# Kernel optimization log

Measured on AMD Instinct MI355X. Metric: run time of the kernel, lower is better.

Reference implementation:

```python
import jax, jax.numpy as jnp
import numpy as np

D_MODEL = 2048
N_HEADS = 16
N_KV_HEADS = 4
D_HEAD = 128
MAX_SEQ_LEN = 4096
RANK = 32
GAMMA_INIT = 0.05
ROPE_BASE = 10000.0


def setup_inputs() -> dict:
    key = jax.random.key(0)
    ks = jax.random.split(key, 10)
    B, T = 1, 2048
    s = lambda fan_in: 1.0 / np.sqrt(fan_in)
    x = jax.random.normal(ks[0], (B, T, D_MODEL), dtype=jnp.float32)
    Wq = jax.random.normal(ks[1], (D_MODEL, N_HEADS * D_HEAD), dtype=jnp.float32) * s(D_MODEL)
    Wk = jax.random.normal(ks[2], (D_MODEL, N_KV_HEADS * D_HEAD), dtype=jnp.float32) * s(D_MODEL)
    Wv = jax.random.normal(ks[3], (D_MODEL, N_KV_HEADS * D_HEAD), dtype=jnp.float32) * s(D_MODEL)
    Wo = jax.random.normal(ks[4], (N_HEADS * D_HEAD, D_MODEL), dtype=jnp.float32) * s(N_HEADS * D_HEAD)
    pol_dir = jax.random.normal(ks[5], (N_HEADS,), dtype=jnp.float32) * 0.1
    pol_WA = jax.random.normal(ks[6], (D_MODEL, RANK), dtype=jnp.float32) * s(D_MODEL)
    pol_WB = jax.random.normal(ks[7], (D_MODEL, RANK), dtype=jnp.float32) * s(D_MODEL)
    pol_gate = jnp.full((N_HEADS,), -3.0, dtype=jnp.float32)
    # gtp_gamma initialized so softplus(gtp_gamma) == geometric ALiBi-style gamma schedule
    slopes = np.linspace(3.0, -3.0, N_HEADS)
    gamma_t = np.clip(GAMMA_INIT * 2.0 ** slopes, 1e-4, None)
    gtp_gamma = jnp.asarray(np.log(np.expm1(gamma_t)), dtype=jnp.float32)
    return {"x": x, "Wq": Wq, "Wk": Wk, "Wv": Wv, "Wo": Wo,
            "pol_dir": pol_dir, "pol_WA": pol_WA, "pol_WB": pol_WB,
            "pol_gate": pol_gate, "gtp_gamma": gtp_gamma}


def _rope(x, offset=0):
    # x: [B,H,T,D]; standard rotate-half RoPE
    B, H, T, D = x.shape
    inv_freq = 1.0 / (ROPE_BASE ** (jnp.arange(0, D, 2, dtype=jnp.float32) / D))
    pos = jnp.arange(T, dtype=jnp.float32) + offset
    ang = pos[:, None] * inv_freq[None, :]          # [T, D/2]
    cos = jnp.cos(ang)[None, None]                  # [1,1,T,D/2]
    sin = jnp.sin(ang)[None, None]
    x1, x2 = x[..., : D // 2], x[..., D // 2 :]
    return jnp.concatenate([x1 * cos - x2 * sin, x2 * cos + x1 * sin], axis=-1)


def reference(x, Wq, Wk, Wv, Wo, pol_dir, pol_WA, pol_WB, pol_gate, gtp_gamma):
    B, T, _ = x.shape
    H, Hkv, D = N_HEADS, N_KV_HEADS, D_HEAD
    n_rep = H // Hkv
    Q = (x @ Wq).reshape(B, T, H, D).transpose(0, 2, 1, 3)     # [B,H,T,D]
    K = (x @ Wk).reshape(B, T, Hkv, D).transpose(0, 2, 1, 3)   # [B,Hkv,T,D]
    V = (x @ Wv).reshape(B, T, Hkv, D).transpose(0, 2, 1, 3)
    Q = _rope(Q)
    K = _rope(K)
    K = jnp.repeat(K, n_rep, axis=1)                           # [B,H,T,D]
    V = jnp.repeat(V, n_rep, axis=1)

    # ---- attention bias ----
    idx = jnp.arange(T)
    delta = (idx[:, None] - idx[None, :]).astype(jnp.float32)  # [T,T], i - j
    causal = delta >= 0
    pol = jnp.clip(pol_dir, -1.0, 1.0)
    polarity_bias = -pol[:, None, None] * (delta / float(MAX_SEQ_LEN))[None]     # [H,T,T]
    gamma = jnp.maximum(jax.nn.softplus(gtp_gamma), 1e-6)
    gtp_bias = -gamma[:, None, None] * jnp.maximum(delta, 0.0)[None]             # [H,T,T]
    bias = (polarity_bias + gtp_bias)[None]                                      # [1,H,T,T]
    # low-rank content-dependent sigmoid bilinear term (prefill: q_len == k_len)
    A = x @ pol_WA                                                               # [B,T,r]
    Bm = x @ pol_WB                                                              # [B,T,r]
    M = jax.nn.sigmoid(jnp.einsum('bir,bjr->bij', A, Bm))                        # [B,T,T]
    gate = jax.nn.sigmoid(pol_gate)[None, :, None, None]
    bias = bias + gate * M[:, None]                                              # [B,H,T,T]
    neg_inf = jnp.finfo(bias.dtype).min
    bias = jnp.where(causal[None, None], bias, neg_inf)

    # ---- SDPA ----
    scores = jnp.einsum('bhid,bhjd->bhij', Q, K) / jnp.sqrt(jnp.float32(D)) + bias
    attn = jax.nn.softmax(scores, axis=-1)
    out = jnp.einsum('bhij,bhjd->bhid', attn, V)                                 # [B,H,T,D]
    out = out.transpose(0, 2, 1, 3).reshape(B, T, H * D)
    return out @ Wo
```

## Files before the change

### kernel.cpp

```cpp
#include <hip/hip_runtime.h>
#include <math.h>

typedef short bf16x8 __attribute__((ext_vector_type(8)));
typedef float f32x4  __attribute__((ext_vector_type(4)));

#define MFMA16 __builtin_amdgcn_mfma_f32_16x16x32_bf16
#define LOG2E 1.4426950408889634f

static __device__ __forceinline__ short f2bf(float f) {
  union { float f; unsigned u; } x; x.f = f;
  unsigned r = (x.u + 0x7FFFu + ((x.u >> 16) & 1u)) >> 16;
  return (short)r;
}
static __device__ __forceinline__ unsigned packbf(float a, float b) {
  return (unsigned)(unsigned short)f2bf(a) | ((unsigned)(unsigned short)f2bf(b) << 16);
}
static __device__ __forceinline__ float bf2f(short s) {
  union { unsigned u; float f; } x; x.u = ((unsigned)(unsigned short)s) << 16;
  return x.f;
}
static __device__ __forceinline__ void gload_lds16(const void* g, void* l) {
  __builtin_amdgcn_global_load_lds((const __attribute__((address_space(1))) void*)g,
                                   (__attribute__((address_space(3))) void*)l, 16, 0, 0);
}
static __device__ __forceinline__ float ex2(float x) {
  float r; asm("v_exp_f32 %0, %1" : "=v"(r) : "v"(x)); return r;
}
static __device__ __forceinline__ float rcpf(float x) {
  float r; asm("v_rcp_f32 %0, %1" : "=v"(r) : "v"(x)); return r;
}
static __device__ __forceinline__ unsigned cvtpk(float lo, float hi) {
  unsigned r; asm("v_cvt_pk_bf16_f32 %0, %1, %2" : "=v"(r) : "v"(lo), "v"(hi));
  return r;
}

__device__ __forceinline__ void tr_tile(
    const float* __restrict__ in, short* __restrict__ out,
    int K, int N, int nt, int kt, float (*t)[33])
{
  int n0 = nt * 32, k0 = kt * 32;
  int tx = threadIdx.x & 31, ty = threadIdx.x >> 5;
  #pragma unroll
  for (int i = 0; i < 4; ++i)
    t[ty + 8 * i][tx] = in[(size_t)(k0 + ty + 8 * i) * N + n0 + tx];
  __syncthreads();
  #pragma unroll
  for (int i = 0; i < 4; ++i)
    out[(size_t)(n0 + ty + 8 * i) * K + k0 + tx] = f2bf(t[tx][ty + 8 * i]);
}

__global__ __launch_bounds__(256) void prep_kernel(
    const float* __restrict__ x, const float* __restrict__ Wq,
    const float* __restrict__ Wk, const float* __restrict__ Wv,
    const float* __restrict__ WA, const float* __restrict__ WB,
    short* __restrict__ xb, short* __restrict__ Wqt, short* __restrict__ Wkt,
    short* __restrict__ Wvt, short* __restrict__ WABt)
{
  __shared__ float t[32][33];
  int b = blockIdx.x;
  if (b < 4096)       tr_tile(Wq, Wqt, 2048, 2048, b & 63, b >> 6, t);
  else if (b < 5120)  { int c = b - 4096; tr_tile(Wk, Wkt, 2048, 512, c & 15, c >> 4, t); }
  else if (b < 6144)  { int c = b - 5120; tr_tile(Wv, Wvt, 2048, 512, c & 15, c >> 4, t); }
  else if (b < 6208)  { int c = b - 6144; tr_tile(WA, WABt, 2048, 32, 0, c, t); }
  else if (b < 6272)  { int c = b - 6208; tr_tile(WB, WABt + 32 * 2048, 2048, 32, 0, c, t); }
  else {
    int i = (b - 6272) * 256 + threadIdx.x;
    float4 v = ((const float4*)x)[i];
    short4 o; o.x = f2bf(v.x); o.y = f2bf(v.y); o.z = f2bf(v.z); o.w = f2bf(v.w);
    ((short4*)xb)[i] = o;
  }
}

__global__ __launch_bounds__(256) void mid_kernel(
    const float* __restrict__ Wo, short* __restrict__ Wot,
    short* __restrict__ Q, short* __restrict__ K)
{
  __shared__ float t[32][33];
  int b = blockIdx.x;
  if (b < 4096) { tr_tile(Wo, Wot, 2048, 2048, b & 63, b >> 6, t); return; }
  int idx = (b - 4096) * 256 + threadIdx.x;
  int d  = idx & 63;
  int hh = (idx >> 6) % 20;
  int tt = idx / (20 * 64);
  short* base = (hh < 16) ? Q + (size_t)tt * 2048 + hh * 128 + d
                          : K + (size_t)tt * 512 + (hh - 16) * 128 + d;
  float inv = __expf((float)d * -0.14391156831212789f);
  float ang = (float)tt * inv;
  float sn, cs;
  __sincosf(ang, &sn, &cs);
  float x1 = bf2f(base[0]), x2 = bf2f(base[64]);
  base[0]  = f2bf(x1 * cs - x2 * sn);
  base[64] = f2bf(x2 * cs + x1 * sn);
}

__device__ __forceinline__ void gemm128_core(
    const short* __restrict__ A, const short* __restrict__ Bt,
    int m0, int n0, int Kd, short* Asm, short* Bsm, f32x4 acc[4][4])
{
  const int tid = threadIdx.x;
  const int lane = tid & 63, w = tid >> 6;
  const int lr = lane & 15, g4 = lane >> 4;
  const int wm = w >> 1, wn = w & 1;

  for (int k0 = 0; k0 < Kd; k0 += 32) {
    #pragma unroll
    for (int s = 0; s < 2; ++s) {
      int c = (s * 4 + w) * 64 + lane;
      int row = c >> 2, q = c & 3;
      gload_lds16(A  + (size_t)(m0 + row) * Kd + k0 + q * 8,
                  Asm + (size_t)(s * 4 + w) * 64 * 8);
      gload_lds16(Bt + (size_t)(n0 + row) * Kd + k0 + q * 8,
                  Bsm + (size_t)(s * 4 + w) * 64 * 8);
    }
    __syncthreads();
    bf16x8 af[4], bff[4];
    #pragma unroll
    for (int mi = 0; mi < 4; ++mi)
      af[mi] = *(const bf16x8*)(Asm + (wm * 64 + mi * 16 + lr) * 32 + g4 * 8);
    #pragma unroll
    for (int ni = 0; ni < 4; ++ni)
      bff[ni] = *(const bf16x8*)(Bsm + (wn * 64 + ni * 16 + lr) * 32 + g4 * 8);
    #pragma unroll
    for (int mi = 0; mi < 4; ++mi)
      #pragma unroll
      for (int ni = 0; ni < 4; ++ni)
        acc[mi][ni] = MFMA16(af[mi], bff[ni], acc[mi][ni], 0, 0, 0);
    __syncthreads();
  }
}

__global__ __launch_bounds__(256, 3) void gemm_qkv_kernel(
    const short* __restrict__ xb, const short* __restrict__ Wqt,
    const short* __restrict__ Wkt, const short* __restrict__ Wvt,
    const short* __restrict__ WABt,
    short* __restrict__ Qb, short* __restrict__ Kb, short* __restrict__ Vtb,
    short* __restrict__ Ab, short* __restrict__ Bb)
{
  __shared__ __align__(16) short Asm[128 * 32];
  __shared__ __align__(16) short Bsm[128 * 32];
  f32x4 acc[4][4];
  #pragma unroll
  for (int i = 0; i < 4; ++i)
    #pragma unroll
    for (int j = 0; j < 4; ++j) acc[i][j] = (f32x4){0.f, 0.f, 0.f, 0.f};

  const int bx = blockIdx.x, by = blockIdx.y;
  const short* Bt; int mode, nl0;
  if (bx < 16)      { Bt = Wqt;  nl0 = bx * 128;        mode = 0; }
  else if (bx < 20) { Bt = Wkt;  nl0 = (bx - 16) * 128; mode = 1; }
  else if (bx < 24) { Bt = Wvt;  nl0 = (bx - 20) * 128; mode = 2; }
  else              { Bt = WABt; nl0 = 0;               mode = 3; }

  gemm128_core(xb, Bt, by * 128, nl0, 2048, Asm, Bsm, acc);

  const int tid = threadIdx.x, lane = tid & 63, w = tid >> 6;
  const int lr = lane & 15, g4 = lane >> 4, wm = w >> 1, wn = w & 1;
  #pragma unroll
  for (int mi = 0; mi < 4; ++mi) {
    #pragma unroll
    for (int ni = 0; ni < 4; ++ni) {
      int mb = by * 128 + wm * 64 + mi * 16 + g4 * 4;
      int nc = nl0 + wn * 64 + ni * 16 + lr;
      if (mode == 0) {
        #pragma unroll
        for (int r = 0; r < 4; ++r)
          Qb[(size_t)(mb + r) * 2048 + nc] = f2bf(acc[mi][ni][r]);
      } else if (mode == 1) {
        #pragma unroll
        for (int r = 0; r < 4; ++r)
          Kb[(size_t)(mb + r) * 512 + nc] = f2bf(acc[mi][ni][r]);
      } else if (mode == 2) {
        uint2 uu;
        uu.x = packbf(acc[mi][ni][0], acc[mi][ni][1]);
        uu.y = packbf(acc[mi][ni][2], acc[mi][ni][3]);
        *(uint2*)(Vtb + (size_t)nc * 2048 + mb) = uu;
      } else {
        if (wn == 0) {
          int col = ni * 16 + lr;
          #pragma unroll
          for (int r = 0; r < 4; ++r) {
            float sv = acc[mi][ni][r];
            if (col < 32) {
              Ab[(size_t)(mb + r) * 32 + col] = f2bf(sv * LOG2E);
            } else {
              Bb[(size_t)(mb + r) * 32 + (col - 32)] = f2bf(sv);
            }
          }
        }
      }
    }
  }
}

__global__ __launch_bounds__(256, 3) void gemm_out_kernel(
    const short* __restrict__ AO, const short* __restrict__ Wot,
    float* __restrict__ out)
{
  __shared__ __align__(16) short Asm[128 * 32];
  __shared__ __align__(16) short Bsm[128 * 32];
  f32x4 acc[4][4];
  #pragma unroll
  for (int i = 0; i < 4; ++i)
    #pragma unroll
    for (int j = 0; j < 4; ++j) acc[i][j] = (f32x4){0.f, 0.f, 0.f, 0.f};

  gemm128_core(AO, Wot, blockIdx.y * 128, blockIdx.x * 128, 2048, Asm, Bsm, acc);

  const int tid = threadIdx.x, lane = tid & 63, w = tid >> 6;
  const int lr = lane & 15, g4 = lane >> 4, wm = w >> 1, wn = w & 1;
  #pragma unroll
  for (int mi = 0; mi < 4; ++mi)
    #pragma unroll
    for (int ni = 0; ni < 4; ++ni) {
      int mb = blockIdx.y * 128 + wm * 64 + mi * 16 + g4 * 4;
      int nc = blockIdx.x * 128 + wn * 64 + ni * 16 + lr;
      #pragma unroll
      for (int r = 0; r < 4; ++r)
        out[(size_t)(mb + r) * 2048 + nc] = acc[mi][ni][r];
    }
}

__global__ __launch_bounds__(256, 2) void attn_kernel(
    const short* __restrict__ Qg, const short* __restrict__ Kg,
    const short* __restrict__ Vtg, const short* __restrict__ Ag,
    const short* __restrict__ Bg, const float* __restrict__ pol_dir,
    const float* __restrict__ pol_gate, const float* __restrict__ gtp_gamma,
    short* __restrict__ AO)
{
  __shared__ __align__(16) char lds[67584];
  char* const Vs = lds + 32768;
  char* const Ps = lds + 49152;

  const int tid = threadIdx.x;
  const int lane = tid & 63, w = tid >> 6;
  const int lr = lane & 15, g4 = lane >> 4;
  const int h  = blockIdx.x;
  const int by = blockIdx.y;
  const int qt = (by < 16) ? (31 - by) : (by - 16);
  const int q0 = qt * 64;
  const int kvh = h >> 2;
  const short* Kh = Kg + kvh * 128;
  const short* Vh = Vtg + (size_t)(kvh * 128) * 2048;

  float pol   = fminf(fmaxf(pol_dir[h], -1.f), 1.f);
  float gamma = fmaxf(log1pf(__expf(gtp_gamma[h])), 1e-6f);
  float gate  = (1.f / (1.f + __expf(-pol_gate[h]))) * LOG2E;
  const float c_h  = -(pol * (1.f / 4096.f) + gamma) * LOG2E;
  const float c16  = 16.f * c_h;
  const float chr1 = c_h, chr2 = c_h + c_h, chr3 = chr2 + c_h;
  const float sc = 0.08838834764831845f * LOG2E;
  const f32x4 z4 = {0.f, 0.f, 0.f, 0.f};

  #pragma unroll
  for (int s = 0; s < 4; ++s) {
    int idx = (w * 4 + s) * 64 + lane;
    int row = idx >> 4, slot = idx & 15;
    gload_lds16(Kh + (size_t)row * 512 + (slot ^ (row & 7)) * 8,
                lds + (w * 4 + s) * 1024);
  }
  #pragma unroll
  for (int s = 0; s < 4; ++s) {
    int idx = (w * 4 + s) * 64 + lane;
    int row = idx >> 3, slot = idx & 7;
    gload_lds16(Vh + (size_t)row * 2048 + (slot ^ (row & 7)) * 8,
                Vs + (w * 4 + s) * 1024);
  }
  #pragma unroll
  for (int s = 0; s < 4; ++s) {
    int c = tid + s * 256;
    int row = c >> 4, sl = c & 15;
    int4 v = *(const int4*)(Qg + (size_t)(q0 + row) * 2048 + h * 128 + sl * 8);
    *(int4*)(lds + 16384 + row * 256 + ((sl * 16) ^ ((row & 7) << 4))) = v;
  }
  {
    int row = tid >> 2, sl = tid & 3;
    int4 va = *(const int4*)(Ag + (size_t)(q0 + row) * 32 + sl * 8);
    *(int4*)(Ps + row * 80 + sl * 16) = va;
    int4 vb = *(const int4*)(Bg + (size_t)row * 32 + sl * 8);
    *(int4*)(lds + 57344 + row * 80 + sl * 16) = vb;
  }
  asm volatile("s_waitcnt vmcnt(0) lgkmcnt(0)" ::: "memory");
  __builtin_amdgcn_s_barrier();

  bf16x8 qf[4];
  #pragma unroll
  for (int kk = 0; kk < 4; ++kk)
    qf[kk] = *(const bf16x8*)(lds + 16384 + (w * 16 + lr) * 256 +
                              ((kk * 64 + g4 * 16) ^ ((lr & 7) << 4)));
  bf16x8 afr = *(const bf16x8*)(Ps + (w * 16 + lr) * 80 + g4 * 16);
  asm volatile("s_waitcnt lgkmcnt(0)" ::: "memory");
  __builtin_amdgcn_s_barrier();

  f32x4 acc_o[8];
  #pragma unroll
  for (int i = 0; i < 8; ++i) acc_o[i] = z4;
  float m_st = -INFINITY, l_st = 0.f;
  char* Pw = Ps + w * 2048;

  for (int jt = 0; jt <= qt; ++jt) {
    const int j0 = jt * 64;
    const bool pf = (jt < qt);
    char* Kcur = lds + ((jt & 1) << 14);
    char* Knxt = lds + (((jt + 1) & 1) << 14);
    char* Bcur = lds + 57344 + (jt & 1) * 5120;
    char* Bnxt = lds + 57344 + ((jt + 1) & 1) * 5120;

    int4 breg;
    if (pf) {
      int brow = tid >> 2, bsl = tid & 3;
      breg = *(const int4*)(Bg + (size_t)(j0 + 64 + brow) * 32 + bsl * 8);
      #pragma unroll
      for (int s = 0; s < 4; ++s) {
        int idx = (w * 4 + s) * 64 + lane;
        int row = idx >> 4, slot = idx & 15;
        gload_lds16(Kh + (size_t)(j0 + 64 + row) * 512 + (slot ^ (row & 7)) * 8,
                    Knxt + (w * 4 + s) * 1024);
      }
    }

    f32x4 acc_s[4], md4[4];
    __builtin_amdgcn_s_setprio(1);
    #pragma unroll
    for (int cb = 0; cb < 4; ++cb) {
      acc_s[cb] = z4;
      #pragma unroll
      for (int kk = 0; kk < 4; ++kk) {
        bf16x8 kf = *(const bf16x8*)(Kcur + (cb * 16 + lr) * 256 +
                                     ((kk * 64 + g4 * 16) ^ ((lr & 7) << 4)));
        acc_s[cb] = MFMA16(kf, qf[kk], acc_s[cb], 0, 0, 0);
      }
      bf16x8 bmf = *(const bf16x8*)(Bcur + (cb * 16 + lr) * 80 + g4 * 16);
      md4[cb] = MFMA16(bmf, afr, z4, 0, 0, 0);
    }
    __builtin_amdgcn_s_setprio(0);

    const int dq = q0 + w * 16 + lr - j0;
    float bq = c_h * (float)(dq - g4 * 4);
    #pragma unroll
    for (int cb = 0; cb < 4; ++cb) {
      float bcb = bq - c16 * (float)cb;
      float sig0 = rcpf(1.f + ex2(-md4[cb][0]));
      float sig1 = rcpf(1.f + ex2(-md4[cb][1]));
      float sig2 = rcpf(1.f + ex2(-md4[cb][2]));
      float sig3 = rcpf(1.f + ex2(-md4[cb][3]));
      acc_s[cb][0] = fmaf(acc_s[cb][0], sc, fmaf(gate, sig0, bcb));
      acc_s[cb][1] = fmaf(acc_s[cb][1], sc, fmaf(gate, sig1, bcb - chr1));
      acc_s[cb][2] = fmaf(acc_s[cb][2], sc, fmaf(gate, sig2, bcb - chr2));
      acc_s[cb][3] = fmaf(acc_s[cb][3], sc, fmaf(gate, sig3, bcb - chr3));
    }
    if (jt == qt) {
      #pragma unroll
      for (int cb = 0; cb < 4; ++cb)
        #pragma unroll
        for (int r = 0; r < 4; ++r)
          if (cb * 16 + g4 * 4 + r > dq) acc_s[cb][r] = -INFINITY;
    }

    float t0 = fmaxf(fmaxf(acc_s[0][0], acc_s[0][1]), acc_s[0][2]);
    float t1 = fmaxf(fmaxf(acc_s[0][3], acc_s[1][0]), acc_s[1][1]);
    float t2 = fmaxf(fmaxf(acc_s[1][2], acc_s[1][3]), acc_s[2][0]);
    float t3 = fmaxf(fmaxf(acc_s[2][1], acc_s[2][2]), acc_s[2][3]);
    float t4 = fmaxf(fmaxf(acc_s[3][0], acc_s[3][1]), acc_s[3][2]);
    float mx = fmaxf(fmaxf(fmaxf(t0, t1), t2),
                     fmaxf(fmaxf(t3, t4), acc_s[3][3]));
    mx = fmaxf(mx, __shfl_xor(mx, 16));
    mx = fmaxf(mx, __shfl_xor(mx, 32));
    if (!__all(mx - m_st <= 11.5415603f)) {
      float mn = fmaxf(m_st, mx);
      float es = ex2(m_st - mn);
      l_st *= es;
      m_st = mn;
      float es4[4];
      #pragma unroll
      for (int r = 0; r < 4; ++r) es4[r] = __shfl(es, g4 * 4 + r, 64);
      #pragma unroll
      for (int db = 0; db < 8; ++db)
        #pragma unroll
        for (int r = 0; r < 4; ++r) acc_o[db][r] *= es4[r];
    }
    float rs = 0.f;
    #pragma unroll
    for (int cb = 0; cb < 4; ++cb)
      #pragma unroll
      for (int r = 0; r < 4; ++r) {
        float p = ex2(acc_s[cb][r] - m_st);
        acc_s[cb][r] = p;
        rs += p;
      }
    rs += __shfl_xor(rs, 16);
    rs += __shfl_xor(rs, 32);
    l_st += rs;

    #pragma unroll
    for (int cb = 0; cb < 4; ++cb) {
      uint2 uu;
      uu.x = cvtpk(acc_s[cb][0], acc_s[cb][1]);
      uu.y = cvtpk(acc_s[cb][2], acc_s[cb][3]);
      *(uint2*)(Pw + lr * 128 + ((cb * 32 + g4 * 8) ^ ((lr & 7) << 4))) = uu;
    }
    asm volatile("s_waitcnt lgkmcnt(0)" ::: "memory");
    if (pf) asm volatile("s_waitcnt vmcnt(5)" ::: "memory");
    else    asm volatile("s_waitcnt vmcnt(0)" ::: "memory");
    __builtin_amdgcn_s_barrier();
    __builtin_amdgcn_sched_barrier(0);

    __builtin_amdgcn_s_setprio(1);
    #pragma unroll
    for (int kk = 0; kk < 2; ++kk) {
      bf16x8 pfr = *(const bf16x8*)(Pw + lr * 128 +
                                    ((kk * 64 + g4 * 16) ^ ((lr & 7) << 4)));
      #pragma unroll
      for (int db = 0; db < 8; ++db) {
        bf16x8 vf = *(const bf16x8*)(Vs + (db * 16 + lr) * 128 +
                                     ((kk * 64 + g4 * 16) ^ ((lr & 7) << 4)));
        acc_o[db] = MFMA16(pfr, vf, acc_o[db], 0, 0, 0);
      }
    }
    __builtin_amdgcn_s_setprio(0);
    __builtin_amdgcn_sched_barrier(0);

    if (pf) {
      int brow = tid >> 2, bsl = tid & 3;
      *(int4*)(Bnxt + brow * 80 + bsl * 16) = breg;
    }
    asm volatile("s_waitcnt vmcnt(0) lgkmcnt(0)" ::: "memory");
    __builtin_amdgcn_s_barrier();
    if (pf) {
      #pragma unroll
      for (int s = 0; s < 4; ++s) {
        int idx = (w * 4 + s) * 64 + lane;
        int row = idx >> 3, slot = idx & 7;
        gload_lds16(Vh + (size_t)row * 2048 + (j0 + 64) + (slot ^ (row & 7)) * 8,
                    Vs + (w * 4 + s) * 1024);
      }
    }
  }

  float lrcp[4];
  #pragma unroll
  for (int r = 0; r < 4; ++r) lrcp[r] = 1.f / __shfl(l_st, g4 * 4 + r, 64);
  #pragma unroll
  for (int db = 0; db < 8; ++db)
    #pragma unroll
    for (int r = 0; r < 4; ++r)
      AO[(size_t)(q0 + w * 16 + g4 * 4 + r) * 2048 + h * 128 + db * 16 + lr] =
          f2bf(acc_o[db][r] * lrcp[r]);
}

extern "C" void kernel_launch(void* const* d_in, const int* in_sizes, int n_in,
                              void* d_out, int out_size, void* d_ws, size_t ws_size,
                              hipStream_t stream) {
  const float* x         = (const float*)d_in[0];
  const float* Wq        = (const float*)d_in[1];
  const float* Wk        = (const float*)d_in[2];
  const float* Wv        = (const float*)d_in[3];
  const float* Wo        = (const float*)d_in[4];
  const float* pol_dir   = (const float*)d_in[5];
  const float* pol_WA    = (const float*)d_in[6];
  const float* pol_WB    = (const float*)d_in[7];
  const float* pol_gate  = (const float*)d_in[8];
  const float* gtp_gamma = (const float*)d_in[9];
  float* out = (float*)d_out;

  char* ws = (char*)d_ws;
  short* Qb   = (short*)(ws);
  short* Kb   = (short*)(ws + 8388608);
  short* Vtb  = (short*)(ws + 10485760);
  short* Ab   = (short*)(ws + 12582912);
  short* Bb   = (short*)(ws + 12713984);
  short* xb   = (short*)(ws + 12845056);
  short* Wot  = xb;
  short* Wqt  = (short*)(ws + 21233664);
  short* AO   = Wqt;
  short* Wkt  = (short*)(ws + 29622272);
  short* Wvt  = (short*)(ws + 31719424);
  short* WABt = (short*)(ws + 33816576);

  prep_kernel<<<10368, 256, 0, stream>>>(x, Wq, Wk, Wv, pol_WA, pol_WB,
                                         xb, Wqt, Wkt, Wvt, WABt);
  gemm_qkv_kernel<<<dim3(25, 16), 256, 0, stream>>>(xb, Wqt, Wkt, Wvt, WABt,
                                                    Qb, Kb, Vtb, Ab, Bb);
  mid_kernel<<<14336, 256, 0, stream>>>(Wo, Wot, Qb, Kb);
  attn_kernel<<<dim3(16, 32), 256, 0, stream>>>(Qb, Kb, Vtb, Ab, Bb,
                                                pol_dir, pol_gate, gtp_gamma, AO);
  gemm_out_kernel<<<dim3(16, 16), 256, 0, stream>>>(AO, Wot, out);
}
```

Baseline: 171.2 us.

## Double-buffer GEMM LDS tiles and shrink attention LDS footprint for occupancy

The shared GEMM core now double-buffers its A/B LDS tiles, prefetching the next K-slice while the current one is multiplied. This replaces the load-then-wait pattern with one barrier per step. The attention kernel drops its separate P and B LDS regions: B fragments are held in registers loaded straight from global memory, and P is written into the consumed K buffer. That cuts LDS from 66KB to 48KB so launch bounds can rise to 3 blocks per SM. The trade-off is more LDS in the GEMMs, extra barriers, fragile vmcnt accounting, and higher register pressure in attention under the tighter occupancy bound.

```diff
diff --git a/kernel.cpp b/kernel.cpp
--- a/kernel.cpp
+++ b/kernel.cpp
@@ -95,37 +95,52 @@
 
 __device__ __forceinline__ void gemm128_core(
     const short* __restrict__ A, const short* __restrict__ Bt,
-    int m0, int n0, int Kd, short* Asm, short* Bsm, f32x4 acc[4][4])
+    int m0, int n0, int Kd, short (*Asm)[4096], short (*Bsm)[4096],
+    f32x4 acc[4][4])
 {
   const int tid = threadIdx.x;
   const int lane = tid & 63, w = tid >> 6;
   const int lr = lane & 15, g4 = lane >> 4;
   const int wm = w >> 1, wn = w & 1;
 
+  #pragma unroll
+  for (int s = 0; s < 2; ++s) {
+    int c = (s * 4 + w) * 64 + lane;
+    int row = c >> 2, q = c & 3;
+    gload_lds16(A  + (size_t)(m0 + row) * Kd + q * 8, Asm[0] + c * 8);
+    gload_lds16(Bt + (size_t)(n0 + row) * Kd + q * 8, Bsm[0] + c * 8);
+  }
+  asm volatile("s_waitcnt vmcnt(0)" ::: "memory");
+  __builtin_amdgcn_s_barrier();
+
   for (int k0 = 0; k0 < Kd; k0 += 32) {
-    #pragma unroll
-    for (int s = 0; s < 2; ++s) {
-      int c = (s * 4 + w) * 64 + lane;
-      int row = c >> 2, q = c & 3;
-      gload_lds16(A  + (size_t)(m0 + row) * Kd + k0 + q * 8,
-                  Asm + (size_t)(s * 4 + w) * 64 * 8);
-      gload_lds16(Bt + (size_t)(n0 + row) * Kd + k0 + q * 8,
-                  Bsm + (size_t)(s * 4 + w) * 64 * 8);
-    }
-    __syncthreads();
+    const int b = (k0 >> 5) & 1;
+    const bool pf = (k0 + 32 < Kd);
+    if (pf) {
+      #pragma unroll
+      for (int s = 0; s < 2; ++s) {
+        int c = (s * 4 + w) * 64 + lane;
+        int row = c >> 2, q = c & 3;
+        gload_lds16(A  + (size_t)(m0 + row) * Kd + k0 + 32 + q * 8,
+                    Asm[b ^ 1] + c * 8);
+        gload_lds16(Bt + (size_t)(n0 + row) * Kd + k0 + 32 + q * 8,
+                    Bsm[b ^ 1] + c * 8);
+      }
+    }
     bf16x8 af[4], bff[4];
     #pragma unroll
     for (int mi = 0; mi < 4; ++mi)
-      af[mi] = *(const bf16x8*)(Asm + (wm * 64 + mi * 16 + lr) * 32 + g4 * 8);
+      af[mi] = *(const bf16x8*)(Asm[b] + (wm * 64 + mi * 16 + lr) * 32 + g4 * 8);
     #pragma unroll
     for (int ni = 0; ni < 4; ++ni)
-      bff[ni] = *(const bf16x8*)(Bsm + (wn * 64 + ni * 16 + lr) * 32 + g4 * 8);
+      bff[ni] = *(const bf16x8*)(Bsm[b] + (wn * 64 + ni * 16 + lr) * 32 + g4 * 8);
     #pragma unroll
     for (int mi = 0; mi < 4; ++mi)
       #pragma unroll
       for (int ni = 0; ni < 4; ++ni)
         acc[mi][ni] = MFMA16(af[mi], bff[ni], acc[mi][ni], 0, 0, 0);
-    __syncthreads();
+    asm volatile("s_waitcnt vmcnt(0) lgkmcnt(0)" ::: "memory");
+    __builtin_amdgcn_s_barrier();
   }
 }
 
@@ -136,8 +151,8 @@
     short* __restrict__ Qb, short* __restrict__ Kb, short* __restrict__ Vtb,
     short* __restrict__ Ab, short* __restrict__ Bb)
 {
-  __shared__ __align__(16) short Asm[128 * 32];
-  __shared__ __align__(16) short Bsm[128 * 32];
+  __shared__ __align__(16) short Asm[2][4096];
+  __shared__ __align__(16) short Bsm[2][4096];
   f32x4 acc[4][4];
   #pragma unroll
   for (int i = 0; i < 4; ++i)
@@ -196,8 +211,8 @@
     const short* __restrict__ AO, const short* __restrict__ Wot,
     float* __restrict__ out)
 {
-  __shared__ __align__(16) short Asm[128 * 32];
-  __shared__ __align__(16) short Bsm[128 * 32];
+  __shared__ __align__(16) short Asm[2][4096];
+  __shared__ __align__(16) short Bsm[2][4096];
   f32x4 acc[4][4];
   #pragma unroll
   for (int i = 0; i < 4; ++i)
@@ -220,16 +235,15 @@
     }
 }
 
-__global__ __launch_bounds__(256, 2) void attn_kernel(
+__global__ __launch_bounds__(256, 3) void attn_kernel(
     const short* __restrict__ Qg, const short* __restrict__ Kg,
     const short* __restrict__ Vtg, const short* __restrict__ Ag,
     const short* __restrict__ Bg, const float* __restrict__ pol_dir,
     const float* __restrict__ pol_gate, const float* __restrict__ gtp_gamma,
     short* __restrict__ AO)
 {
-  __shared__ __align__(16) char lds[67584];
+  __shared__ __align__(16) char lds[49152];
   char* const Vs = lds + 32768;
-  char* const Ps = lds + 49152;
 
   const int tid = threadIdx.x;
   const int lane = tid & 63, w = tid >> 6;
@@ -253,11 +267,39 @@
 
   #pragma unroll
   for (int s = 0; s < 4; ++s) {
+    int c = tid + s * 256;
+    int row = c >> 4, sl = c & 15;
+    int4 v = *(const int4*)(Qg + (size_t)(q0 + row) * 2048 + h * 128 + sl * 8);
+    *(int4*)(lds + 16384 + row * 256 + ((sl * 16) ^ ((row & 7) << 4))) = v;
+  }
+  {
+    int row = tid >> 2, sl = tid & 3;
+    int4 va = *(const int4*)(Ag + (size_t)(q0 + row) * 32 + sl * 8);
+    *(int4*)(Vs + row * 80 + sl * 16) = va;
+  }
+  asm volatile("s_waitcnt lgkmcnt(0)" ::: "memory");
+  __builtin_amdgcn_s_barrier();
+
+  bf16x8 qf[4];
+  #pragma unroll
+  for (int kk = 0; kk < 4; ++kk)
+    qf[kk] = *(const bf16x8*)(lds + 16384 + (w * 16 + lr) * 256 +
+                              ((kk * 64 + g4 * 16) ^ ((lr & 7) << 4)));
+  bf16x8 afr = *(const bf16x8*)(Vs + (w * 16 + lr) * 80 + g4 * 16);
+  asm volatile("s_waitcnt lgkmcnt(0)" ::: "memory");
+  __builtin_amdgcn_s_barrier();
+
+  #pragma unroll
+  for (int s = 0; s < 4; ++s) {
     int idx = (w * 4 + s) * 64 + lane;
     int row = idx >> 4, slot = idx & 15;
     gload_lds16(Kh + (size_t)row * 512 + (slot ^ (row & 7)) * 8,
                 lds + (w * 4 + s) * 1024);
   }
+  bf16x8 bcur[4];
+  #pragma unroll
+  for (int cb = 0; cb < 4; ++cb)
+    bcur[cb] = *(const bf16x8*)(Bg + (size_t)(cb * 16 + lr) * 32 + g4 * 8);
   #pragma unroll
   for (int s = 0; s < 4; ++s) {
     int idx = (w * 4 + s) * 64 + lane;
@@ -265,50 +307,19 @@
     gload_lds16(Vh + (size_t)row * 2048 + (slot ^ (row & 7)) * 8,
                 Vs + (w * 4 + s) * 1024);
   }
-  #pragma unroll
-  for (int s = 0; s < 4; ++s) {
-    int c = tid + s * 256;
-    int row = c >> 4, sl = c & 15;
-    int4 v = *(const int4*)(Qg + (size_t)(q0 + row) * 2048 + h * 128 + sl * 8);
-    *(int4*)(lds + 16384 + row * 256 + ((sl * 16) ^ ((row & 7) << 4))) = v;
-  }
-  {
-    int row = tid >> 2, sl = tid & 3;
-    int4 va = *(const int4*)(Ag + (size_t)(q0 + row) * 32 + sl * 8);
-    *(int4*)(Ps + row * 80 + sl * 16) = va;
-    int4 vb = *(const int4*)(Bg + (size_t)row * 32 + sl * 8);
-    *(int4*)(lds + 57344 + row * 80 + sl * 16) = vb;
-  }
-  asm volatile("s_waitcnt vmcnt(0) lgkmcnt(0)" ::: "memory");
-  __builtin_amdgcn_s_barrier();
-
-  bf16x8 qf[4];
-  #pragma unroll
-  for (int kk = 0; kk < 4; ++kk)
-    qf[kk] = *(const bf16x8*)(lds + 16384 + (w * 16 + lr) * 256 +
-                              ((kk * 64 + g4 * 16) ^ ((lr & 7) << 4)));
-  bf16x8 afr = *(const bf16x8*)(Ps + (w * 16 + lr) * 80 + g4 * 16);
-  asm volatile("s_waitcnt lgkmcnt(0)" ::: "memory");
-  __builtin_amdgcn_s_barrier();
 
   f32x4 acc_o[8];
   #pragma unroll
   for (int i = 0; i < 8; ++i) acc_o[i] = z4;
   float m_st = -INFINITY, l_st = 0.f;
-  char* Pw = Ps + w * 2048;
 
   for (int jt = 0; jt <= qt; ++jt) {
     const int j0 = jt * 64;
     const bool pf = (jt < qt);
     char* Kcur = lds + ((jt & 1) << 14);
     char* Knxt = lds + (((jt + 1) & 1) << 14);
-    char* Bcur = lds + 57344 + (jt & 1) * 5120;
-    char* Bnxt = lds + 57344 + ((jt + 1) & 1) * 5120;
-
-    int4 breg;
+
     if (pf) {
-      int brow = tid >> 2, bsl = tid & 3;
-      breg = *(const int4*)(Bg + (size_t)(j0 + 64 + brow) * 32 + bsl * 8);
       #pragma unroll
       for (int s = 0; s < 4; ++s) {
         int idx = (w * 4 + s) * 64 + lane;
@@ -317,6 +328,9 @@
                     Knxt + (w * 4 + s) * 1024);
       }
     }
+    if (pf) asm volatile("s_waitcnt vmcnt(8)" ::: "memory");
+    else    asm volatile("s_waitcnt vmcnt(4)" ::: "memory");
+    __builtin_amdgcn_s_barrier();
 
     f32x4 acc_s[4], md4[4];
     __builtin_amdgcn_s_setprio(1);
@@ -329,10 +343,16 @@
                                      ((kk * 64 + g4 * 16) ^ ((lr & 7) << 4)));
         acc_s[cb] = MFMA16(kf, qf[kk], acc_s[cb], 0, 0, 0);
       }
-      bf16x8 bmf = *(const bf16x8*)(Bcur + (cb * 16 + lr) * 80 + g4 * 16);
-      md4[cb] = MFMA16(bmf, afr, z4, 0, 0, 0);
+      md4[cb] = MFMA16(bcur[cb], afr, z4, 0, 0, 0);
     }
     __builtin_amdgcn_s_setprio(0);
+
+    if (pf) {
+      #pragma unroll
+      for (int cb = 0; cb < 4; ++cb)
+        bcur[cb] = *(const bf16x8*)(Bg + (size_t)(j0 + 64 + cb * 16 + lr) * 32 +
+                                    g4 * 8);
+    }
 
     const int dq = q0 + w * 16 + lr - j0;
     float bq = c_h * (float)(dq - g4 * 4);
@@ -391,6 +411,11 @@
     rs += __shfl_xor(rs, 32);
     l_st += rs;
 
+    if (pf) asm volatile("s_waitcnt vmcnt(8)" ::: "memory");
+    else    asm volatile("s_waitcnt vmcnt(0)" ::: "memory");
+    __builtin_amdgcn_s_barrier();
+
+    char* Pw = Kcur + w * 2048;
     #pragma unroll
     for (int cb = 0; cb < 4; ++cb) {
       uint2 uu;
@@ -399,11 +424,7 @@
       *(uint2*)(Pw + lr * 128 + ((cb * 32 + g4 * 8) ^ ((lr & 7) << 4))) = uu;
     }
     asm volatile("s_waitcnt lgkmcnt(0)" ::: "memory");
-    if (pf) asm volatile("s_waitcnt vmcnt(5)" ::: "memory");
-    else    asm volatile("s_waitcnt vmcnt(0)" ::: "memory");
-    __builtin_amdgcn_s_barrier();
     __builtin_amdgcn_sched_barrier(0);
-
     __builtin_amdgcn_s_setprio(1);
     #pragma unroll
     for (int kk = 0; kk < 2; ++kk) {
@@ -419,11 +440,6 @@
     __builtin_amdgcn_s_setprio(0);
     __builtin_amdgcn_sched_barrier(0);
 
-    if (pf) {
-      int brow = tid >> 2, bsl = tid & 3;
-      *(int4*)(Bnxt + brow * 80 + bsl * 16) = breg;
-    }
-    asm volatile("s_waitcnt vmcnt(0) lgkmcnt(0)" ::: "memory");
     __builtin_amdgcn_s_barrier();
     if (pf) {
       #pragma unroll
```

Result: slower. 184.8 us (+7.9%).
